# Optimization experiments

Hardware: AMD Instinct MI355X
Metric: run time of the kernel (lower is better)

The kernel has to match this reference:

```python
import jax, jax.numpy as jnp
import numpy as np

N_NODES = 100_000
N_EDGES = 1_600_000
N_GRAPHS = 512
NF = 64        # n_node_feats
H1 = 128       # hidden width
H2 = 64        # dim_node_emb
DIM_OUT = 1
STEPS = 4      # set2set processing steps


def _lin(x, W, b):
    # torch Linear convention: y = x @ W.T + b, W: [out, in]
    return x @ W.T + b


def _gelu(x):
    return jax.nn.gelu(x, approximate=False)  # torch.nn.GELU default (erf)


def _lstm_cell(x, h, c, Wih, Whh, bih, bhh):
    g = x @ Wih.T + bih + h @ Whh.T + bhh
    i, f, gg, o = jnp.split(g, 4, axis=-1)  # torch gate order: i, f, g, o
    i, f, o = jax.nn.sigmoid(i), jax.nn.sigmoid(f), jax.nn.sigmoid(o)
    gg = jnp.tanh(gg)
    c = f * c + i * gg
    h = o * jnp.tanh(c)
    return h, c


def setup_inputs() -> dict:
    key = jax.random.key(0)
    ks = jax.random.split(key, 24)
    p = lambda k, shp: jax.random.normal(k, shp, dtype=jnp.float32) * 0.05
    inp = {
        "x": jax.random.normal(ks[0], (N_NODES, NF), dtype=jnp.float32),
        "edge_index": jax.random.randint(ks[1], (2, N_EDGES), 0, N_NODES, dtype=jnp.int32),
        "batch": jnp.sort(jax.random.randint(ks[2], (N_NODES,), 0, N_GRAPHS, dtype=jnp.int32)),
        "nfc_W": p(ks[3], (H1, NF)), "nfc_b": p(ks[4], (H1,)),
        "gc1_W": p(ks[5], (H1, H1)), "gc1_b": p(ks[6], (H1,)),
        "gc2_W": p(ks[7], (H2, H1)), "gc2_b": p(ks[8], (H2,)),
        "lstm0_Wih": p(ks[9], (4 * H2, 2 * H2)), "lstm0_Whh": p(ks[10], (4 * H2, H2)),
        "lstm0_bih": p(ks[11], (4 * H2,)), "lstm0_bhh": p(ks[12], (4 * H2,)),
        "lstm1_Wih": p(ks[13], (4 * H2, H2)), "lstm1_Whh": p(ks[14], (4 * H2, H2)),
        "lstm1_bih": p(ks[15], (4 * H2,)), "lstm1_bhh": p(ks[16], (4 * H2,)),
        "fc1_W": p(ks[17], (32, 2 * H2)), "fc1_b": p(ks[18], (32,)),
        "fc2_W": p(ks[19], (DIM_OUT, 32)), "fc2_b": p(ks[20], (DIM_OUT,)),
    }
    return inp


def _forward(x, edge_index, batch, nfc_W, nfc_b, gc1_W, gc1_b, gc2_W, gc2_b,
             lstm0_Wih, lstm0_Whh, lstm0_bih, lstm0_bhh,
             lstm1_Wih, lstm1_Whh, lstm1_bih, lstm1_bhh,
             fc1_W, fc1_b, fc2_W, fc2_b):
    src, dst = edge_index[0], edge_index[1]

    def gin_conv(h, W, b):
        # PyG GINConv, eps=0: lin((1+eps)*x + sum_{j in N(i)} x_j)
        agg = jax.ops.segment_sum(h[src], dst, num_segments=N_NODES)
        return _lin(h + agg, W, b)

    h = _gelu(_lin(x, nfc_W, nfc_b))
    h = _gelu(gin_conv(h, gc1_W, gc1_b))
    h = _gelu(gin_conv(h, gc2_W, gc2_b))
    # F.normalize(p=2, dim=1)
    h = h / jnp.maximum(jnp.linalg.norm(h, axis=1, keepdims=True), 1e-12)

    # Set2Set: 2-layer LSTM, 4 processing steps, scatter-softmax attention
    B = N_GRAPHS
    h0 = jnp.zeros((B, H2), jnp.float32); c0 = jnp.zeros((B, H2), jnp.float32)
    h1 = jnp.zeros((B, H2), jnp.float32); c1 = jnp.zeros((B, H2), jnp.float32)
    q_star = jnp.zeros((B, 2 * H2), jnp.float32)
    for _ in range(STEPS):
        h0, c0 = _lstm_cell(q_star, h0, c0, lstm0_Wih, lstm0_Whh, lstm0_bih, lstm0_bhh)
        h1, c1 = _lstm_cell(h0, h1, c1, lstm1_Wih, lstm1_Whh, lstm1_bih, lstm1_bhh)
        q = h1  # [B, H2]
        e = jnp.sum(h * q[batch], axis=-1, keepdims=True)  # [N, 1]
        m = jax.ops.segment_max(e, batch, num_segments=B)
        ex = jnp.exp(e - m[batch])
        s = jax.ops.segment_sum(ex, batch, num_segments=B)
        a = ex / (s[batch] + 1e-16)
        r = jax.ops.segment_sum(a * h, batch, num_segments=B)  # [B, H2]
        q_star = jnp.concatenate([q, r], axis=-1)

    z = _gelu(_lin(q_star, fc1_W, fc1_b))
    z = _lin(z, fc2_W, fc2_b)
    return z, h


def reference(x, edge_index, batch, nfc_W, nfc_b, gc1_W, gc1_b, gc2_W, gc2_b,
              lstm0_Wih, lstm0_Whh, lstm0_bih, lstm0_bhh,
              lstm1_Wih, lstm1_Whh, lstm1_bih, lstm1_bhh,
              fc1_W, fc1_b, fc2_W, fc2_b):
    return _forward(x, edge_index, batch, nfc_W, nfc_b, gc1_W, gc1_b, gc2_W, gc2_b,
                    lstm0_Wih, lstm0_Whh, lstm0_bih, lstm0_bhh,
                    lstm1_Wih, lstm1_Whh, lstm1_bih, lstm1_bhh,
                    fc1_W, fc1_b, fc2_W, fc2_b)
```

## Files before the change

### kernel.cpp

```cpp
#include <hip/hip_runtime.h>
#include <hip/hip_bf16.h>
#include <math.h>

constexpr int N  = 100000;
constexpr int E  = 1600000;
constexpr int NG = 512;
constexpr int NF = 64;
constexpr int H1 = 128;
constexpr int H2 = 64;

constexpr int BW   = 128;
constexpr int NB   = (N + BW - 1) / BW;
constexpr int CAP  = 2600;
constexpr int CHUNK = 2048;

constexpr int MAXN = 416;
constexpr int RST  = 68;

typedef __attribute__((ext_vector_type(8))) short short8;
typedef __attribute__((ext_vector_type(4))) float f32x4;

__device__ __forceinline__ float gelu_f(float x) {
    return 0.5f * x * (1.0f + erff(x * 0.70710678118654752f));
}
__device__ __forceinline__ float sigmoid_f(float x) {
    return 1.0f / (1.0f + expf(-x));
}
__device__ __forceinline__ float waveAllSum(float v) {
    #pragma unroll
    for (int m = 32; m; m >>= 1) v += __shfl_xor(v, m);
    return v;
}
__device__ __forceinline__ unsigned short f2bf(float x) {
    __hip_bfloat16 b = __float2bfloat16(x);
    return *reinterpret_cast<unsigned short*>(&b);
}
__device__ __forceinline__ float bf2f(unsigned short u) {
    return __uint_as_float(((unsigned int)u) << 16);
}
__device__ __forceinline__ float bf_lo(unsigned int u) { return __uint_as_float(u << 16); }
__device__ __forceinline__ float bf_hi(unsigned int u) { return __uint_as_float(u & 0xffff0000u); }

__device__ __forceinline__ void bfsplit(float v, unsigned short& hi, unsigned short& lo) {
    hi = f2bf(v);
    lo = f2bf(v - bf2f(hi));
}

__global__ __launch_bounds__(256) void setup_kernel(const int* __restrict__ batch,
                                                    const float* __restrict__ Wih0, const float* __restrict__ Whh0,
                                                    const float* __restrict__ bih0, const float* __restrict__ bhh0,
                                                    const float* __restrict__ Wih1, const float* __restrict__ Whh1,
                                                    const float* __restrict__ bih1, const float* __restrict__ bhh1,
                                                    float* __restrict__ WT0, float* __restrict__ WT1,
                                                    float* __restrict__ b0, float* __restrict__ b1,
                                                    int* __restrict__ bcursor, int* __restrict__ gstart) {
    int i = blockIdx.x * 256 + threadIdx.x;
    if (i < 192 * 256) {
        int k = i >> 8, j = i & 255;
        WT0[i] = (k < 128) ? Wih0[j * 128 + k] : Whh0[j * 64 + (k - 128)];
    }
    if (i < 128 * 256) {
        int k = i >> 8, j = i & 255;
        WT1[i] = (k < 64) ? Wih1[j * 64 + k] : Whh1[j * 64 + (k - 64)];
    }
    if (i < 256) { b0[i] = bih0[i] + bhh0[i]; b1[i] = bih1[i] + bhh1[i]; }
    if (i < NB) bcursor[i] = i * CAP;
    if (i <= NG) {
        if (i == NG) gstart[NG] = N;
        else {
            int lo = 0, hi = N;
            while (lo < hi) {
                int mid = (lo + hi) >> 1;
                if (batch[mid] < i) lo = mid + 1; else hi = mid;
            }
            gstart[i] = lo;
        }
    }
}

__global__ __launch_bounds__(256) void bin_scatter_kernel(const int* __restrict__ ei,
                                                          int* __restrict__ bcursor,
                                                          int* __restrict__ pairs) {
    __shared__ int hist[NB];
    __shared__ int start_s[NB];
    __shared__ int lcur[NB];
    int tid = threadIdx.x;
    int e0 = blockIdx.x * CHUNK;
    for (int b = tid; b < NB; b += 256) hist[b] = 0;
    __syncthreads();
    #pragma unroll 4
    for (int k = 0; k < CHUNK / 256; ++k) {
        int e = e0 + k * 256 + tid;
        if (e < E) atomicAdd(&hist[ei[E + e] >> 7], 1);
    }
    __syncthreads();
    for (int b = tid; b < NB; b += 256) {
        if (hist[b]) start_s[b] = atomicAdd(&bcursor[b], hist[b]);
        lcur[b] = 0;
    }
    __syncthreads();
    #pragma unroll 4
    for (int k = 0; k < CHUNK / 256; ++k) {
        int e = e0 + k * 256 + tid;
        if (e < E) {
            int d = ei[E + e];
            int s = ei[e];
            int b = d >> 7;
            int pos = start_s[b] + atomicAdd(&lcur[b], 1);
            if (pos < (b + 1) * CAP) pairs[pos] = (s << 7) | (d & 127);
        }
    }
}

__global__ __launch_bounds__(256) void csr_bucket_kernel(const int* __restrict__ pairs,
                                                         const int* __restrict__ bcursor,
                                                         int* __restrict__ srcs,
                                                         int2* __restrict__ nrange) {
    __shared__ int cnt_l[BW];
    __shared__ int cur_l[BW];
    __shared__ int wt[2];
    int b = blockIdx.x;
    int tid = threadIdx.x;
    int base = b * CAP;
    int cnt = bcursor[b] - base;
    if (cnt > CAP) cnt = CAP;
    if (tid < BW) cnt_l[tid] = 0;
    __syncthreads();
    for (int i = tid; i < cnt; i += 256) {
        atomicAdd(&cnt_l[pairs[base + i] & 127], 1);
    }
    __syncthreads();
    if (tid < BW) {
        int v = cnt_l[tid];
        int lane = tid & 63, w = tid >> 6;
        int incl = v;
        #pragma unroll
        for (int off = 1; off < 64; off <<= 1) {
            int t = __shfl_up(incl, off);
            if (lane >= off) incl += t;
        }
        if (lane == 63) wt[w] = incl;
        __syncthreads();
        int excl = (w ? wt[0] : 0) + incl - v;
        int node = b * BW + tid;
        if (node < N) nrange[node] = make_int2(base + excl, base + excl + v);
        cur_l[tid] = excl;
    } else {
        __syncthreads();
    }
    __syncthreads();
    for (int i = tid; i < cnt; i += 256) {
        int p = pairs[base + i];
        int pos = atomicAdd(&cur_l[p & 127], 1);
        srcs[base + pos] = p >> 7;
    }
}

template <int ID, int OD, int IN_SPLIT, int OUT_MODE>
__global__ __launch_bounds__(256) void lin_mfma_kernel(const void* __restrict__ in_v,
                                                       const float* __restrict__ W,
                                                       const float* __restrict__ bias,
                                                       void* __restrict__ out_v, int nrows) {
    constexpr int KC = 32;
    constexpr int NCH = ID / KC;
    constexpr int AST = 40;
    constexpr int NCT = OD / 16;
    constexpr int LDSU = 2 * 128 * AST + 2 * OD * AST;
    __shared__ __align__(16) unsigned short lds[LDSU];
    unsigned short* Ahi = lds;
    unsigned short* Alo = lds + 128 * AST;
    unsigned short* Whi = lds + 2 * 128 * AST;
    unsigned short* Wlo = lds + 2 * 128 * AST + OD * AST;

    int tid = threadIdx.x;
    int w = tid >> 6, lane = tid & 63;
    int m15 = lane & 15, quad = lane >> 4;
    int nb = blockIdx.x * 128;

    f32x4 acc[2][NCT];
    #pragma unroll
    for (int rt = 0; rt < 2; ++rt)
        #pragma unroll
        for (int ct = 0; ct < NCT; ++ct) acc[rt][ct] = (f32x4)0.f;

    for (int c = 0; c < NCH; ++c) {
        int kb = c * KC;
        if (IN_SPLIT == 0) {
            const float* in = (const float*)in_v;
            #pragma unroll
            for (int it = 0; it < 4; ++it) {
                int f4 = it * 256 + tid;
                int row = f4 >> 3, kq = (f4 & 7) * 4;
                float4 v = make_float4(0.f, 0.f, 0.f, 0.f);
                if (nb + row < nrows) v = *(const float4*)&in[(size_t)(nb + row) * ID + kb + kq];
                unsigned short h0, h1, h2, h3, l0, l1, l2, l3;
                bfsplit(v.x, h0, l0); bfsplit(v.y, h1, l1);
                bfsplit(v.z, h2, l2); bfsplit(v.w, h3, l3);
                uint2 uh, ul;
                uh.x = (unsigned int)h0 | ((unsigned int)h1 << 16);
                uh.y = (unsigned int)h2 | ((unsigned int)h3 << 16);
                ul.x = (unsigned int)l0 | ((unsigned int)l1 << 16);
                ul.y = (unsigned int)l2 | ((unsigned int)l3 << 16);
                *(uint2*)&Ahi[row * AST + kq] = uh;
                *(uint2*)&Alo[row * AST + kq] = ul;
            }
        } else {
            const uint4* in4 = (const uint4*)in_v;
            #pragma unroll
            for (int it = 0; it < 4; ++it) {
                int i = it * 256 + tid;
                int row = i >> 3, grp = i & 7;
                uint4 u = make_uint4(0u, 0u, 0u, 0u);
                if (nb + row < nrows) u = in4[(size_t)(nb + row) * 32 + c * 8 + grp];
                *(uint2*)&Ahi[row * AST + grp * 4] = make_uint2(u.x, u.y);
                *(uint2*)&Alo[row * AST + grp * 4] = make_uint2(u.z, u.w);
            }
        }
        #pragma unroll
        for (int it = 0; it < OD / 32; ++it) {
            int f4 = it * 256 + tid;
            int o = f4 >> 3, kq = (f4 & 7) * 4;
            float4 v = *(const float4*)&W[(size_t)o * ID + kb + kq];
            unsigned short h0, h1, h2, h3, l0, l1, l2, l3;
            bfsplit(v.x, h0, l0); bfsplit(v.y, h1, l1);
            bfsplit(v.z, h2, l2); bfsplit(v.w, h3, l3);
            uint2 uh, ul;
            uh.x = (unsigned int)h0 | ((unsigned int)h1 << 16);
            uh.y = (unsigned int)h2 | ((unsigned int)h3 << 16);
            ul.x = (unsigned int)l0 | ((unsigned int)l1 << 16);
            ul.y = (unsigned int)l2 | ((unsigned int)l3 << 16);
            *(uint2*)&Whi[o * AST + kq] = uh;
            *(uint2*)&Wlo[o * AST + kq] = ul;
        }
        __syncthreads();

        short8 ah0 = *(const short8*)&Ahi[(w * 32 + m15) * AST + quad * 8];
        short8 ah1 = *(const short8*)&Ahi[(w * 32 + 16 + m15) * AST + quad * 8];
        short8 al0 = *(const short8*)&Alo[(w * 32 + m15) * AST + quad * 8];
        short8 al1 = *(const short8*)&Alo[(w * 32 + 16 + m15) * AST + quad * 8];
        #pragma unroll
        for (int ct = 0; ct < NCT; ++ct) {
            short8 bh = *(const short8*)&Whi[(ct * 16 + m15) * AST + quad * 8];
            short8 bl = *(const short8*)&Wlo[(ct * 16 + m15) * AST + quad * 8];
            acc[0][ct] = __builtin_amdgcn_mfma_f32_16x16x32_bf16(ah0, bh, acc[0][ct], 0, 0, 0);
            acc[0][ct] = __builtin_amdgcn_mfma_f32_16x16x32_bf16(ah0, bl, acc[0][ct], 0, 0, 0);
            acc[0][ct] = __builtin_amdgcn_mfma_f32_16x16x32_bf16(al0, bh, acc[0][ct], 0, 0, 0);
            acc[1][ct] = __builtin_amdgcn_mfma_f32_16x16x32_bf16(ah1, bh, acc[1][ct], 0, 0, 0);
            acc[1][ct] = __builtin_amdgcn_mfma_f32_16x16x32_bf16(ah1, bl, acc[1][ct], 0, 0, 0);
            acc[1][ct] = __builtin_amdgcn_mfma_f32_16x16x32_bf16(al1, bh, acc[1][ct], 0, 0, 0);
        }
        __syncthreads();
    }

    float bcol[NCT];
    #pragma unroll
    for (int ct = 0; ct < NCT; ++ct) bcol[ct] = bias[ct * 16 + m15];

    if (OUT_MODE == 1) {
        constexpr int EPS = OD + 8;
        unsigned short* ep = lds;
        #pragma unroll
        for (int rt = 0; rt < 2; ++rt)
            #pragma unroll
            for (int ct = 0; ct < NCT; ++ct)
                #pragma unroll
                for (int r = 0; r < 4; ++r) {
                    int rl = w * 32 + rt * 16 + quad * 4 + r;
                    float v = gelu_f(acc[rt][ct][r] + bcol[ct]);
                    ep[rl * EPS + ct * 16 + m15] = f2bf(v);
                }
        __syncthreads();
        constexpr int U4 = 128 * OD / 8;
        for (int i = tid; i < U4; i += 256) {
            int row = i / (OD / 8);
            int off = (i % (OD / 8)) * 8;
            int grow = nb + row;
            if (grow < nrows) {
                uint4 v = *(const uint4*)&ep[row * EPS + off];
                *(uint4*)((unsigned short*)out_v + (size_t)grow * OD + off) = v;
            }
        }
    } else {
        float* out = (float*)out_v;
        #pragma unroll
        for (int rt = 0; rt < 2; ++rt) {
            #pragma unroll
            for (int r = 0; r < 4; ++r) {
                float vv[NCT];
                float ss = 0.f;
                #pragma unroll
                for (int ct = 0; ct < NCT; ++ct) {
                    vv[ct] = gelu_f(acc[rt][ct][r] + bcol[ct]);
                    ss += vv[ct] * vv[ct];
                }
                #pragma unroll
                for (int mm = 1; mm < 16; mm <<= 1) ss += __shfl_xor(ss, mm);
                float denom = fmaxf(sqrtf(ss), 1e-12f);
                int grow = nb + w * 32 + rt * 16 + quad * 4 + r;
                if (grow < nrows) {
                    #pragma unroll
                    for (int ct = 0; ct < NCT; ++ct)
                        out[(size_t)grow * OD + ct * 16 + m15] = vv[ct] / denom;
                }
            }
        }
    }
}

__global__ __launch_bounds__(256) void agg_kernel(const uint2* __restrict__ hb2,
                                                  const int2* __restrict__ nrange,
                                                  const int* __restrict__ srcs,
                                                  uint4* __restrict__ utab) {
    int wave = threadIdx.x >> 6, lane = threadIdx.x & 63;
    int half = lane >> 5, hl = lane & 31;
    int n = blockIdx.x * 4 + wave;
    if (n >= N) return;
    int2 rng = nrange[n];
    int s0 = rng.x, deg = rng.y - rng.x;
    int m1 = deg < 64 ? deg : 64;
    int pre = (lane < m1) ? srcs[s0 + lane] : 0;
    float a0 = 0.f, a1 = 0.f, a2 = 0.f, a3 = 0.f;
    int t = 0;
    for (; t + 8 <= m1; t += 8) {
        int i0 = __shfl(pre, t + half);
        int i1 = __shfl(pre, t + 2 + half);
        int i2 = __shfl(pre, t + 4 + half);
        int i3 = __shfl(pre, t + 6 + half);
        uint2 u0 = hb2[(size_t)i0 * 32 + hl];
        uint2 u1 = hb2[(size_t)i1 * 32 + hl];
        uint2 u2 = hb2[(size_t)i2 * 32 + hl];
        uint2 u3 = hb2[(size_t)i3 * 32 + hl];
        a0 += bf_lo(u0.x); a1 += bf_hi(u0.x); a2 += bf_lo(u0.y); a3 += bf_hi(u0.y);
        a0 += bf_lo(u1.x); a1 += bf_hi(u1.x); a2 += bf_lo(u1.y); a3 += bf_hi(u1.y);
        a0 += bf_lo(u2.x); a1 += bf_hi(u2.x); a2 += bf_lo(u2.y); a3 += bf_hi(u2.y);
        a0 += bf_lo(u3.x); a1 += bf_hi(u3.x); a2 += bf_lo(u3.y); a3 += bf_hi(u3.y);
    }
    for (; t < m1; t += 2) {
        int idx = t + half;
        int idc = idx < m1 ? idx : 0;
        int s = __shfl(pre, idc);
        if (idx < m1) {
            uint2 u = hb2[(size_t)s * 32 + hl];
            a0 += bf_lo(u.x); a1 += bf_hi(u.x); a2 += bf_lo(u.y); a3 += bf_hi(u.y);
        }
    }
    for (int j = 64 + half; j < deg; j += 2) {
        int s = srcs[s0 + j];
        uint2 u = hb2[(size_t)s * 32 + hl];
        a0 += bf_lo(u.x); a1 += bf_hi(u.x); a2 += bf_lo(u.y); a3 += bf_hi(u.y);
    }
    a0 += __shfl_down(a0, 32);
    a1 += __shfl_down(a1, 32);
    a2 += __shfl_down(a2, 32);
    a3 += __shfl_down(a3, 32);
    if (half == 0) {
        uint2 u = hb2[(size_t)n * 32 + hl];
        a0 += bf_lo(u.x); a1 += bf_hi(u.x); a2 += bf_lo(u.y); a3 += bf_hi(u.y);
        unsigned short h0, h1, h2, h3, l0, l1, l2, l3;
        bfsplit(a0, h0, l0); bfsplit(a1, h1, l1);
        bfsplit(a2, h2, l2); bfsplit(a3, h3, l3);
        uint4 o;
        o.x = (unsigned int)h0 | ((unsigned int)h1 << 16);
        o.y = (unsigned int)h2 | ((unsigned int)h3 << 16);
        o.z = (unsigned int)l0 | ((unsigned int)l1 << 16);
        o.w = (unsigned int)l2 | ((unsigned int)l3 << 16);
        utab[(size_t)n * 32 + hl] = o;
    }
}

__global__ __launch_bounds__(256) void set2set_kernel(const float* __restrict__ hn,
                                                      const int* __restrict__ gstart,
                                                      const float* __restrict__ WT0, const float* __restrict__ b0,
                                                      const float* __restrict__ WT1, const float* __restrict__ b1,
                                                      float* __restrict__ qstar_out) {
    __shared__ __align__(16) unsigned short hL[MAXN * RST];
    __shared__ float av[MAXN];
    __shared__ __align__(16) float xc0[192];
    __shared__ __align__(16) float xc1[128];
    __shared__ __align__(16) float gates[256];
    __shared__ float c0v[H2], c1v[H2];
    __shared__ float red[4];
    __shared__ float rp[4][H2];
    __shared__ float sp[4];

    int g = blockIdx.x;
    int tid = threadIdx.x, w = tid >> 6, lane = tid & 63;
    int s0 = gstart[g], s1 = gstart[g + 1];
    int cnt = s1 - s0;
    int cL = cnt < MAXN ? cnt : MAXN;
    const float* hq = xc1 + 64;

    for (int idx = tid; idx < cL * 16; idx += 256) {
        int n = idx >> 4, p4 = idx & 15;
        float4 v = *(const float4*)&hn[(size_t)(s0 + n) * 64 + p4 * 4];
        uint2 u;
        u.x = (unsigned int)f2bf(v.x) | ((unsigned int)f2bf(v.y) << 16);
        u.y = (unsigned int)f2bf(v.z) | ((unsigned int)f2bf(v.w) << 16);
        *(uint2*)&hL[n * RST + p4 * 4] = u;
    }
    if (tid < 192) xc0[tid] = 0.f;
    if (tid < 128) xc1[tid] = 0.f;
    if (tid < H2) { c0v[tid] = 0.f; c1v[tid] = 0.f; }
    float b0v = b0[tid], b1v = b1[tid];
    __syncthreads();

    for (int step = 0; step < 4; ++step) {
        {
            float a0 = 0.f, a1 = 0.f, a2 = 0.f, a3 = 0.f;
            #pragma unroll 8
            for (int k = 0; k < 192; k += 4) {
                a0 += xc0[k]     * WT0[(k)     * 256 + tid];
                a1 += xc0[k + 1] * WT0[(k + 1) * 256 + tid];
                a2 += xc0[k + 2] * WT0[(k + 2) * 256 + tid];
                a3 += xc0[k + 3] * WT0[(k + 3) * 256 + tid];
            }
            gates[tid] = (a0 + a1) + (a2 + a3) + b0v;
        }
        __syncthreads();
        if (tid < H2) {
            float ii = sigmoid_f(gates[tid]), ff = sigmoid_f(gates[H2 + tid]);
            float gg = tanhf(gates[2 * H2 + tid]), oo = sigmoid_f(gates[3 * H2 + tid]);
            float c = ff * c0v[tid] + ii * gg;
            float h = oo * tanhf(c);
            c0v[tid] = c; xc0[128 + tid] = h; xc1[tid] = h;
        }
        __syncthreads();
        {
            float a0 = 0.f, a1 = 0.f, a2 = 0.f, a3 = 0.f;
            #pragma unroll 8
            for (int k = 0; k < 128; k += 4) {
                a0 += xc1[k]     * WT1[(k)     * 256 + tid];
                a1 += xc1[k + 1] * WT1[(k + 1) * 256 + tid];
                a2 += xc1[k + 2] * WT1[(k + 2) * 256 + tid];
                a3 += xc1[k + 3] * WT1[(k + 3) * 256 + tid];
            }
            gates[tid] = (a0 + a1) + (a2 + a3) + b1v;
        }
        __syncthreads();
        if (tid < H2) {
            float ii = sigmoid_f(gates[tid]), ff = sigmoid_f(gates[H2 + tid]);
            float gg = tanhf(gates[2 * H2 + tid]), oo = sigmoid_f(gates[3 * H2 + tid]);
            float c = ff * c1v[tid] + ii * gg;
            float h = oo * tanhf(c);
            c1v[tid] = c; xc1[64 + tid] = h;
        }
        __syncthreads();

        float lm = -INFINITY;
        for (int i = tid; i < cnt; i += 256) {
            float e = 0.f;
            if (i < MAXN) {
                const uint2* row = (const uint2*)&hL[i * RST];
                #pragma unroll
                for (int p4 = 0; p4 < 16; ++p4) {
                    uint2 u = row[p4];
                    e += bf_lo(u.x) * hq[p4 * 4 + 0];
                    e += bf_hi(u.x) * hq[p4 * 4 + 1];
                    e += bf_lo(u.y) * hq[p4 * 4 + 2];
                    e += bf_hi(u.y) * hq[p4 * 4 + 3];
                }
                av[i] = e;
            } else {
                for (int f = 0; f < 64; ++f) e += hn[(size_t)(s0 + i) * 64 + f] * hq[f];
            }
            lm = fmaxf(lm, e);
        }
        #pragma unroll
        for (int mm = 32; mm; mm >>= 1) lm = fmaxf(lm, __shfl_xor(lm, mm));
        if (lane == 0) red[w] = lm;
        __syncthreads();
        float m = fmaxf(fmaxf(red[0], red[1]), fmaxf(red[2], red[3]));

        float ps = 0.f;
        for (int i = tid; i < cnt; i += 256) {
            float e;
            if (i < MAXN) e = av[i];
            else {
                e = 0.f;
                for (int f = 0; f < 64; ++f) e += hn[(size_t)(s0 + i) * 64 + f] * hq[f];
            }
            float p = expf(e - m);
            ps += p;
            if (i < MAXN) av[i] = p;
        }
        ps = waveAllSum(ps);
        if (lane == 0) sp[w] = ps;
        __syncthreads();
        float s = sp[0] + sp[1] + sp[2] + sp[3];

        float racc = 0.f;
        for (int i = w; i < cL; i += 4) {
            unsigned short hv = hL[i * RST + lane];
            racc += av[i] * bf2f(hv);
        }
        float qf = hq[lane];
        for (int n = MAXN + w; n < cnt; n += 4) {
            float v = hn[(size_t)(s0 + n) * 64 + lane];
            float e = waveAllSum(v * qf);
            float p = expf(e - m);
            racc += p * v;
        }
        rp[w][lane] = racc;
        __syncthreads();
        if (tid < H2) {
            float r = 0.f;
            if (cnt > 0) {
                r = (rp[0][tid] + rp[1][tid] + rp[2][tid] + rp[3][tid]) / (s + 1e-16f);
            }
            xc0[tid] = xc1[64 + tid];
            xc0[H2 + tid] = r;
        }
        __syncthreads();
    }
    if (tid < 2 * H2) qstar_out[g * 2 * H2 + tid] = xc0[tid];
}

__global__ __launch_bounds__(256) void fcout_kernel(const float* __restrict__ q_star,
                                                    const float* __restrict__ W1, const float* __restrict__ b1,
                                                    const float* __restrict__ W2, const float* __restrict__ b2,
                                                    float* __restrict__ z) {
    __shared__ float W1l[32 * 128];
    __shared__ float b1l[32], W2l[32];
    int tid = threadIdx.x;
    for (int i = tid; i < 32 * 128; i += 256) W1l[i] = W1[i];
    if (tid < 32) { b1l[tid] = b1[tid]; W2l[tid] = W2[tid]; }
    __syncthreads();
    int g = blockIdx.x * 256 + tid;
    float acc[32];
    #pragma unroll
    for (int j = 0; j < 32; ++j) acc[j] = b1l[j];
    for (int k = 0; k < 128; ++k) {
        float qv = q_star[g * 128 + k];
        #pragma unroll
        for (int j = 0; j < 32; ++j) acc[j] += qv * W1l[j * 128 + k];
    }
    float zv = b2[0];
    #pragma unroll
    for (int j = 0; j < 32; ++j) zv += gelu_f(acc[j]) * W2l[j];
    z[g] = zv;
}

extern "C" void kernel_launch(void* const* d_in, const int* in_sizes, int n_in,
                              void* d_out, int out_size, void* d_ws, size_t ws_size,
                              hipStream_t stream) {
    const float* x       = (const float*)d_in[0];
    const int*   ei      = (const int*)d_in[1];
    const int*   batch   = (const int*)d_in[2];
    const float* nfc_W   = (const float*)d_in[3];
    const float* nfc_b   = (const float*)d_in[4];
    const float* gc1_W   = (const float*)d_in[5];
    const float* gc1_b   = (const float*)d_in[6];
    const float* gc2_W   = (const float*)d_in[7];
    const float* gc2_b   = (const float*)d_in[8];
    const float* l0_Wih  = (const float*)d_in[9];
    const float* l0_Whh  = (const float*)d_in[10];
    const float* l0_bih  = (const float*)d_in[11];
    const float* l0_bhh  = (const float*)d_in[12];
    const float* l1_Wih  = (const float*)d_in[13];
    const float* l1_Whh  = (const float*)d_in[14];
    const float* l1_bih  = (const float*)d_in[15];
    const float* l1_bhh  = (const float*)d_in[16];
    const float* fc1_W   = (const float*)d_in[17];
    const float* fc1_b   = (const float*)d_in[18];
    const float* fc2_W   = (const float*)d_in[19];
    const float* fc2_b   = (const float*)d_in[20];

    float* out = (float*)d_out;
    float* hn_out = out + NG;

    char* p = (char*)d_ws;
    auto take = [&](size_t bytes) {
        char* r = p;
        p += (bytes + 255) & ~size_t(255);
        return r;
    };
    float*        sbuf  = (float*)take((size_t)N * H1 * 4);
    unsigned int* hbbuf = (unsigned int*)take((size_t)N * H1 * 2);
    int*   srcs   = (int*)take((size_t)NB * CAP * 4);
    int2*  nrange = (int2*)take((size_t)N * 8);
    int*   bcursor= (int*)take((size_t)NB * 4);
    int*   gstart = (int*)take((size_t)(NG + 1) * 4);
    float* qstar  = (float*)take((size_t)NG * 2 * H2 * 4);
    float* WT0    = (float*)take((size_t)192 * 256 * 4);
    float* WT1    = (float*)take((size_t)128 * 256 * 4);
    float* b0     = (float*)take((size_t)256 * 4);
    float* b1     = (float*)take((size_t)256 * 4);

    int* pairs = (int*)sbuf;

    setup_kernel<<<192, 256, 0, stream>>>(batch, l0_Wih, l0_Whh, l0_bih, l0_bhh,
                                          l1_Wih, l1_Whh, l1_bih, l1_bhh,
                                          WT0, WT1, b0, b1, bcursor, gstart);

    bin_scatter_kernel<<<(E + CHUNK - 1) / CHUNK, 256, 0, stream>>>(ei, bcursor, pairs);
    csr_bucket_kernel<<<NB, 256, 0, stream>>>(pairs, bcursor, srcs, nrange);

    int mfmaGrid = (N + 127) / 128;
    lin_mfma_kernel<NF, H1, 0, 1><<<mfmaGrid, 256, 0, stream>>>(x, nfc_W, nfc_b, hbbuf, N);
    agg_kernel<<<(N + 3) / 4, 256, 0, stream>>>((const uint2*)hbbuf, nrange, srcs, (uint4*)sbuf);
    lin_mfma_kernel<H1, H1, 1, 1><<<mfmaGrid, 256, 0, stream>>>(sbuf, gc1_W, gc1_b, hbbuf, N);
    agg_kernel<<<(N + 3) / 4, 256, 0, stream>>>((const uint2*)hbbuf, nrange, srcs, (uint4*)sbuf);
    lin_mfma_kernel<H1, H2, 1, 2><<<mfmaGrid, 256, 0, stream>>>(sbuf, gc2_W, gc2_b, hn_out, N);

    set2set_kernel<<<NG, 256, 0, stream>>>(hn_out, gstart, WT0, b0, WT1, b1, qstar);

    fcout_kernel<<<2, 256, 0, stream>>>(qstar, fc1_W, fc1_b, fc2_W, fc2_b, out);
}
```

Baseline: 474.6 us.

## Reorder second GIN conv to project before aggregation and fuse both linears

Uses the linearity of the second GIN layer: the 128-wide hidden features are multiplied by gc2_W first, and the 64-wide projection is then aggregated over neighbours. That halves the gather width of the second aggregation and removes one full-size intermediate pass. The gc1 and gc2 matmuls now run in one kernel that writes the projection in fp16, and a new aggregation kernel applies the bias, GELU and L2 normalisation. Storing the aggregated values in fp16 may cost accuracy, and the bin-scatter CHUNK size is also doubled.

```diff
diff --git a/kernel.cpp b/kernel.cpp
--- a/kernel.cpp
+++ b/kernel.cpp
@@ -1,5 +1,6 @@
 #include <hip/hip_runtime.h>
 #include <hip/hip_bf16.h>
+#include <hip/hip_fp16.h>
 #include <math.h>
 
 constexpr int N  = 100000;
@@ -12,7 +13,7 @@
 constexpr int BW   = 128;
 constexpr int NB   = (N + BW - 1) / BW;
 constexpr int CAP  = 2600;
-constexpr int CHUNK = 2048;
+constexpr int CHUNK = 4096;
 
 constexpr int MAXN = 416;
 constexpr int RST  = 68;
@@ -156,11 +157,11 @@
     }
 }
 
-template <int ID, int OD, int IN_SPLIT, int OUT_MODE>
-__global__ __launch_bounds__(256) void lin_mfma_kernel(const void* __restrict__ in_v,
+template <int ID, int OD>
+__global__ __launch_bounds__(256) void lin_mfma_kernel(const float* __restrict__ in,
                                                        const float* __restrict__ W,
                                                        const float* __restrict__ bias,
-                                                       void* __restrict__ out_v, int nrows) {
+                                                       unsigned short* __restrict__ out_bf, int nrows) {
     constexpr int KC = 32;
     constexpr int NCH = ID / KC;
     constexpr int AST = 40;
@@ -185,36 +186,22 @@
 
     for (int c = 0; c < NCH; ++c) {
         int kb = c * KC;
-        if (IN_SPLIT == 0) {
-            const float* in = (const float*)in_v;
-            #pragma unroll
-            for (int it = 0; it < 4; ++it) {
-                int f4 = it * 256 + tid;
-                int row = f4 >> 3, kq = (f4 & 7) * 4;
-                float4 v = make_float4(0.f, 0.f, 0.f, 0.f);
-                if (nb + row < nrows) v = *(const float4*)&in[(size_t)(nb + row) * ID + kb + kq];
-                unsigned short h0, h1, h2, h3, l0, l1, l2, l3;
-                bfsplit(v.x, h0, l0); bfsplit(v.y, h1, l1);
-                bfsplit(v.z, h2, l2); bfsplit(v.w, h3, l3);
-                uint2 uh, ul;
-                uh.x = (unsigned int)h0 | ((unsigned int)h1 << 16);
-                uh.y = (unsigned int)h2 | ((unsigned int)h3 << 16);
-                ul.x = (unsigned int)l0 | ((unsigned int)l1 << 16);
-                ul.y = (unsigned int)l2 | ((unsigned int)l3 << 16);
-                *(uint2*)&Ahi[row * AST + kq] = uh;
-                *(uint2*)&Alo[row * AST + kq] = ul;
-            }
-        } else {
-            const uint4* in4 = (const uint4*)in_v;
-            #pragma unroll
-            for (int it = 0; it < 4; ++it) {
-                int i = it * 256 + tid;
-                int row = i >> 3, grp = i & 7;
-                uint4 u = make_uint4(0u, 0u, 0u, 0u);
-                if (nb + row < nrows) u = in4[(size_t)(nb + row) * 32 + c * 8 + grp];
-                *(uint2*)&Ahi[row * AST + grp * 4] = make_uint2(u.x, u.y);
-                *(uint2*)&Alo[row * AST + grp * 4] = make_uint2(u.z, u.w);
-            }
+        #pragma unroll
+        for (int it = 0; it < 4; ++it) {
+            int f4 = it * 256 + tid;
+            int row = f4 >> 3, kq = (f4 & 7) * 4;
+            float4 v = make_float4(0.f, 0.f, 0.f, 0.f);
+            if (nb + row < nrows) v = *(const float4*)&in[(size_t)(nb + row) * ID + kb + kq];
+            unsigned short h0, h1, h2, h3, l0, l1, l2, l3;
+            bfsplit(v.x, h0, l0); bfsplit(v.y, h1, l1);
+            bfsplit(v.z, h2, l2); bfsplit(v.w, h3, l3);
+            uint2 uh, ul;
+            uh.x = (unsigned int)h0 | ((unsigned int)h1 << 16);
+            uh.y = (unsigned int)h2 | ((unsigned int)h3 << 16);
+            ul.x = (unsigned int)l0 | ((unsigned int)l1 << 16);
+            ul.y = (unsigned int)l2 | ((unsigned int)l3 << 16);
+            *(uint2*)&Ahi[row * AST + kq] = uh;
+            *(uint2*)&Alo[row * AST + kq] = ul;
         }
         #pragma unroll
         for (int it = 0; it < OD / 32; ++it) {
@@ -256,53 +243,27 @@
     #pragma unroll
     for (int ct = 0; ct < NCT; ++ct) bcol[ct] = bias[ct * 16 + m15];
 
-    if (OUT_MODE == 1) {
-        constexpr int EPS = OD + 8;
-        unsigned short* ep = lds;
-        #pragma unroll
-        for (int rt = 0; rt < 2; ++rt)
-            #pragma unroll
-            for (int ct = 0; ct < NCT; ++ct)
-                #pragma unroll
-                for (int r = 0; r < 4; ++r) {
-                    int rl = w * 32 + rt * 16 + quad * 4 + r;
-                    float v = gelu_f(acc[rt][ct][r] + bcol[ct]);
-                    ep[rl * EPS + ct * 16 + m15] = f2bf(v);
-                }
-        __syncthreads();
-        constexpr int U4 = 128 * OD / 8;
-        for (int i = tid; i < U4; i += 256) {
-            int row = i / (OD / 8);
-            int off = (i % (OD / 8)) * 8;
-            int grow = nb + row;
-            if (grow < nrows) {
-                uint4 v = *(const uint4*)&ep[row * EPS + off];
-                *(uint4*)((unsigned short*)out_v + (size_t)grow * OD + off) = v;
-            }
-        }
-    } else {
-        float* out = (float*)out_v;
-        #pragma unroll
-        for (int rt = 0; rt < 2; ++rt) {
+    constexpr int EPS = OD + 8;
+    unsigned short* ep = lds;
+    #pragma unroll
+    for (int rt = 0; rt < 2; ++rt)
+        #pragma unroll
+        for (int ct = 0; ct < NCT; ++ct)
             #pragma unroll
             for (int r = 0; r < 4; ++r) {
-                float vv[NCT];
-                float ss = 0.f;
-                #pragma unroll
-                for (int ct = 0; ct < NCT; ++ct) {
-                    vv[ct] = gelu_f(acc[rt][ct][r] + bcol[ct]);
-                    ss += vv[ct] * vv[ct];
-                }
-                #pragma unroll
-                for (int mm = 1; mm < 16; mm <<= 1) ss += __shfl_xor(ss, mm);
-                float denom = fmaxf(sqrtf(ss), 1e-12f);
-                int grow = nb + w * 32 + rt * 16 + quad * 4 + r;
-                if (grow < nrows) {
-                    #pragma unroll
-                    for (int ct = 0; ct < NCT; ++ct)
-                        out[(size_t)grow * OD + ct * 16 + m15] = vv[ct] / denom;
-                }
-            }
+                int rl = w * 32 + rt * 16 + quad * 4 + r;
+                float v = gelu_f(acc[rt][ct][r] + bcol[ct]);
+                ep[rl * EPS + ct * 16 + m15] = f2bf(v);
+            }
+    __syncthreads();
+    constexpr int U4 = 128 * OD / 8;
+    for (int i = tid; i < U4; i += 256) {
+        int row = i / (OD / 8);
+        int off = (i % (OD / 8)) * 8;
+        int grow = nb + row;
+        if (grow < nrows) {
+            uint4 v = *(const uint4*)&ep[row * EPS + off];
+            *(uint4*)(out_bf + (size_t)grow * OD + off) = v;
         }
     }
 }
@@ -368,6 +329,213 @@
     }
 }
 
+__global__ __launch_bounds__(256) void lin2_fused_kernel(const uint4* __restrict__ in4,
+                                                         const float* __restrict__ W1,
+                                                         const float* __restrict__ b1,
+                                                         const float* __restrict__ W2,
+                                                         unsigned short* __restrict__ y2,
+                                                         int nrows) {
+    constexpr int AST = 40;
+    __shared__ __align__(16) unsigned short lds[4 * 128 * AST];
+    unsigned short* Ahi = lds;
+    unsigned short* Alo = lds + 128 * AST;
+    unsigned short* Whi = lds + 2 * 128 * AST;
+    unsigned short* Wlo = lds + 3 * 128 * AST;
+
+    int tid = threadIdx.x;
+    int w = tid >> 6, lane = tid & 63;
+    int m15 = lane & 15, quad = lane >> 4;
+    int nb = blockIdx.x * 128;
+
+    f32x4 acc[2][8];
+    #pragma unroll
+    for (int rt = 0; rt < 2; ++rt)
+        #pragma unroll
+        for (int ct = 0; ct < 8; ++ct) acc[rt][ct] = (f32x4)0.f;
+
+    for (int c = 0; c < 4; ++c) {
+        #pragma unroll
+        for (int it = 0; it < 4; ++it) {
+            int i = it * 256 + tid;
+            int row = i >> 3, grp = i & 7;
+            uint4 u = make_uint4(0u, 0u, 0u, 0u);
+            if (nb + row < nrows) u = in4[(size_t)(nb + row) * 32 + c * 8 + grp];
+            *(uint2*)&Ahi[row * AST + grp * 4] = make_uint2(u.x, u.y);
+            *(uint2*)&Alo[row * AST + grp * 4] = make_uint2(u.z, u.w);
+        }
+        #pragma unroll
+        for (int it = 0; it < 4; ++it) {
+            int f4 = it * 256 + tid;
+            int o = f4 >> 3, kq = (f4 & 7) * 4;
+            float4 v = *(const float4*)&W1[(size_t)o * 128 + c * 32 + kq];
+            unsigned short h0, h1, h2, h3, l0, l1, l2, l3;
+            bfsplit(v.x, h0, l0); bfsplit(v.y, h1, l1);
+            bfsplit(v.z, h2, l2); bfsplit(v.w, h3, l3);
+            uint2 uh, ul;
+            uh.x = (unsigned int)h0 | ((unsigned int)h1 << 16);
+            uh.y = (unsigned int)h2 | ((unsigned int)h3 << 16);
+            ul.x = (unsigned int)l0 | ((unsigned int)l1 << 16);
+            ul.y = (unsigned int)l2 | ((unsigned int)l3 << 16);
+            *(uint2*)&Whi[o * AST + kq] = uh;
+            *(uint2*)&Wlo[o * AST + kq] = ul;
+        }
+        __syncthreads();
+        short8 ah0 = *(const short8*)&Ahi[(w * 32 + m15) * AST + quad * 8];
+        short8 ah1 = *(const short8*)&Ahi[(w * 32 + 16 + m15) * AST + quad * 8];
+        short8 al0 = *(const short8*)&Alo[(w * 32 + m15) * AST + quad * 8];
+        short8 al1 = *(const short8*)&Alo[(w * 32 + 16 + m15) * AST + quad * 8];
+        #pragma unroll
+        for (int ct = 0; ct < 8; ++ct) {
+            short8 bh = *(const short8*)&Whi[(ct * 16 + m15) * AST + quad * 8];
+            short8 bl = *(const short8*)&Wlo[(ct * 16 + m15) * AST + quad * 8];
+            acc[0][ct] = __builtin_amdgcn_mfma_f32_16x16x32_bf16(ah0, bh, acc[0][ct], 0, 0, 0);
+            acc[0][ct] = __builtin_amdgcn_mfma_f32_16x16x32_bf16(ah0, bl, acc[0][ct], 0, 0, 0);
+            acc[0][ct] = __builtin_amdgcn_mfma_f32_16x16x32_bf16(al0, bh, acc[0][ct], 0, 0, 0);
+            acc[1][ct] = __builtin_amdgcn_mfma_f32_16x16x32_bf16(ah1, bh, acc[1][ct], 0, 0, 0);
+            acc[1][ct] = __builtin_amdgcn_mfma_f32_16x16x32_bf16(ah1, bl, acc[1][ct], 0, 0, 0);
+            acc[1][ct] = __builtin_amdgcn_mfma_f32_16x16x32_bf16(al1, bh, acc[1][ct], 0, 0, 0);
+        }
+        __syncthreads();
+    }
+
+    #pragma unroll
+    for (int ct = 0; ct < 8; ++ct) {
+        float bc = b1[ct * 16 + m15];
+        #pragma unroll
+        for (int rt = 0; rt < 2; ++rt)
+            #pragma unroll
+            for (int r = 0; r < 4; ++r)
+                acc[rt][ct][r] = gelu_f(acc[rt][ct][r] + bc);
+    }
+
+    f32x4 acc2[2][4];
+    #pragma unroll
+    for (int rt = 0; rt < 2; ++rt)
+        #pragma unroll
+        for (int ct = 0; ct < 4; ++ct) acc2[rt][ct] = (f32x4)0.f;
+
+    for (int c2 = 0; c2 < 4; ++c2) {
+        __syncthreads();
+        #pragma unroll
+        for (int rt = 0; rt < 2; ++rt)
+            #pragma unroll
+            for (int cc = 0; cc < 2; ++cc) {
+                int ct = c2 * 2 + cc;
+                #pragma unroll
+                for (int r = 0; r < 4; ++r) {
+                    int node = w * 32 + rt * 16 + quad * 4 + r;
+                    unsigned short hi, lo;
+                    bfsplit(acc[rt][ct][r], hi, lo);
+                    Ahi[node * AST + cc * 16 + m15] = hi;
+                    Alo[node * AST + cc * 16 + m15] = lo;
+                }
+            }
+        #pragma unroll
+        for (int it = 0; it < 2; ++it) {
+            int f4 = it * 256 + tid;
+            int o = f4 >> 3, kq = (f4 & 7) * 4;
+            float4 v = *(const float4*)&W2[(size_t)o * 128 + c2 * 32 + kq];
+            unsigned short h0, h1, h2, h3, l0, l1, l2, l3;
+            bfsplit(v.x, h0, l0); bfsplit(v.y, h1, l1);
+            bfsplit(v.z, h2, l2); bfsplit(v.w, h3, l3);
+            uint2 uh, ul;
+            uh.x = (unsigned int)h0 | ((unsigned int)h1 << 16);
+            uh.y = (unsigned int)h2 | ((unsigned int)h3 << 16);
+            ul.x = (unsigned int)l0 | ((unsigned int)l1 << 16);
+            ul.y = (unsigned int)l2 | ((unsigned int)l3 << 16);
+            *(uint2*)&Whi[o * AST + kq] = uh;
+            *(uint2*)&Wlo[o * AST + kq] = ul;
+        }
+        __syncthreads();
+        short8 ah0 = *(const short8*)&Ahi[(w * 32 + m15) * AST + quad * 8];
+        short8 ah1 = *(const short8*)&Ahi[(w * 32 + 16 + m15) * AST + quad * 8];
+        short8 al0 = *(const short8*)&Alo[(w * 32 + m15) * AST + quad * 8];
+        short8 al1 = *(const short8*)&Alo[(w * 32 + 16 + m15) * AST + quad * 8];
+        #pragma unroll
+        for (int ct = 0; ct < 4; ++ct) {
+            short8 bh = *(const short8*)&Whi[(ct * 16 + m15) * AST + quad * 8];
+            short8 bl = *(const short8*)&Wlo[(ct * 16 + m15) * AST + quad * 8];
+            acc2[0][ct] = __builtin_amdgcn_mfma_f32_16x16x32_bf16(ah0, bh, acc2[0][ct], 0, 0, 0);
+            acc2[0][ct] = __builtin_amdgcn_mfma_f32_16x16x32_bf16(ah0, bl, acc2[0][ct], 0, 0, 0);
+            acc2[0][ct] = __builtin_amdgcn_mfma_f32_16x16x32_bf16(al0, bh, acc2[0][ct], 0, 0, 0);
+            acc2[1][ct] = __builtin_amdgcn_mfma_f32_16x16x32_bf16(ah1, bh, acc2[1][ct], 0, 0, 0);
+            acc2[1][ct] = __builtin_amdgcn_mfma_f32_16x16x32_bf16(ah1, bl, acc2[1][ct], 0, 0, 0);
+            acc2[1][ct] = __builtin_amdgcn_mfma_f32_16x16x32_bf16(al1, bh, acc2[1][ct], 0, 0, 0);
+        }
+    }
+    __syncthreads();
+
+    constexpr int EPS = 72;
+    unsigned short* ep = lds;
+    #pragma unroll
+    for (int rt = 0; rt < 2; ++rt)
+        #pragma unroll
+        for (int ct = 0; ct < 4; ++ct)
+            #pragma unroll
+            for (int r = 0; r < 4; ++r) {
+                int rl = w * 32 + rt * 16 + quad * 4 + r;
+                __half hv = __float2half(acc2[rt][ct][r]);
+                ep[rl * EPS + ct * 16 + m15] = *reinterpret_cast<unsigned short*>(&hv);
+            }
+    __syncthreads();
+    for (int i = tid; i < 1024; i += 256) {
+        int row = i >> 3, off = (i & 7) * 8;
+        int grow = nb + row;
+        if (grow < nrows)
+            *(uint4*)(y2 + (size_t)grow * 64 + off) = *(const uint4*)&ep[row * EPS + off];
+    }
+}
+
+__global__ __launch_bounds__(256) void agg2_norm_kernel(const uint2* __restrict__ y2,
+                                                        const int2* __restrict__ nrange,
+                                                        const int* __restrict__ srcs,
+                                                        const float* __restrict__ b2,
+                                                        float* __restrict__ hn) {
+    int wave = threadIdx.x >> 6, lane = threadIdx.x & 63;
+    int qw = lane >> 4, ql = lane & 15;
+    int n = blockIdx.x * 4 + wave;
+    if (n >= N) return;
+    int2 rng = nrange[n];
+    int s0 = rng.x, deg = rng.y - rng.x;
+    int m1 = deg < 64 ? deg : 64;
+    int pre = (lane < m1) ? srcs[s0 + lane] : 0;
+    float a0 = 0.f, a1 = 0.f, a2 = 0.f, a3 = 0.f;
+    auto addu = [&](uint2 u) {
+        float2 f01 = __half22float2(*reinterpret_cast<__half2*>(&u.x));
+        float2 f23 = __half22float2(*reinterpret_cast<__half2*>(&u.y));
+        a0 += f01.x; a1 += f01.y; a2 += f23.x; a3 += f23.y;
+    };
+    int t = 0;
+    for (; t + 8 <= m1; t += 8) {
+        int i0 = __shfl(pre, t + qw);
+        int i1 = __shfl(pre, t + 4 + qw);
+        uint2 u0 = y2[(size_t)i0 * 16 + ql];
+        uint2 u1 = y2[(size_t)i1 * 16 + ql];
+        addu(u0); addu(u1);
+    }
+    for (; t < m1; t += 4) {
+        int idx = t + qw;
+        int s = __shfl(pre, idx < m1 ? idx : 0);
+        if (idx < m1) addu(y2[(size_t)s * 16 + ql]);
+    }
+    for (int j = 64 + qw; j < deg; j += 4) addu(y2[(size_t)srcs[s0 + j] * 16 + ql]);
+    a0 += __shfl_down(a0, 32); a1 += __shfl_down(a1, 32);
+    a2 += __shfl_down(a2, 32); a3 += __shfl_down(a3, 32);
+    a0 += __shfl_down(a0, 16); a1 += __shfl_down(a1, 16);
+    a2 += __shfl_down(a2, 16); a3 += __shfl_down(a3, 16);
+    if (qw == 0) {
+        addu(y2[(size_t)n * 16 + ql]);
+        float4 bv = *(const float4*)&b2[ql * 4];
+        float v0 = gelu_f(a0 + bv.x), v1 = gelu_f(a1 + bv.y);
+        float v2 = gelu_f(a2 + bv.z), v3 = gelu_f(a3 + bv.w);
+        float ss = v0 * v0 + v1 * v1 + v2 * v2 + v3 * v3;
+        #pragma unroll
+        for (int mm = 1; mm < 16; mm <<= 1) ss += __shfl_xor(ss, mm);
+        float d = fmaxf(sqrtf(ss), 1e-12f);
+        *(float4*)&hn[(size_t)n * 64 + ql * 4] = make_float4(v0 / d, v1 / d, v2 / d, v3 / d);
+    }
+}
+
 __global__ __launch_bounds__(256) void set2set_kernel(const float* __restrict__ hn,
                                                       const int* __restrict__ gstart,
                                                       const float* __restrict__ WT0, const float* __restrict__ b0,
@@ -574,8 +742,8 @@
         p += (bytes + 255) & ~size_t(255);
         return r;
     };
-    float*        sbuf  = (float*)take((size_t)N * H1 * 4);
-    unsigned int* hbbuf = (unsigned int*)take((size_t)N * H1 * 2);
+    float*          sbuf  = (float*)take((size_t)N * H1 * 4);
+    unsigned short* hbbuf = (unsigned short*)take((size_t)N * H1 * 2);
     int*   srcs   = (int*)take((size_t)NB * CAP * 4);
     int2*  nrange = (int2*)take((size_t)N * 8);
     int*   bcursor= (int*)take((size_t)NB * 4);
@@ -596,11 +764,12 @@
     csr_bucket_kernel<<<NB, 256, 0, stream>>>(pairs, bcursor, srcs, nrange);
 
     int mfmaGrid = (N + 127) / 128;
-    lin_mfma_kernel<NF, H1, 0, 1><<<mfmaGrid, 256, 0, stream>>>(x, nfc_W, nfc_b, hbbuf, N);
+    lin_mfma_kernel<NF, H1><<<mfmaGrid, 256, 0, stream>>>(x, nfc_W, nfc_b, hbbuf, N);
     agg_kernel<<<(N + 3) / 4, 256, 0, stream>>>((const uint2*)hbbuf, nrange, srcs, (uint4*)sbuf);
-    lin_mfma_kernel<H1, H1, 1, 1><<<mfmaGrid, 256, 0, stream>>>(sbuf, gc1_W, gc1_b, hbbuf, N);
-    agg_kernel<<<(N + 3) / 4, 256, 0, stream>>>((const uint2*)hbbuf, nrange, srcs, (uint4*)sbuf);
-    lin_mfma_kernel<H1, H2, 1, 2><<<mfmaGrid, 256, 0, stream>>>(sbuf, gc2_W, gc2_b, hn_out, N);
+    lin2_fused_kernel<<<mfmaGrid, 256, 0, stream>>>((const uint4*)sbuf, gc1_W, gc1_b, gc2_W,
+                                                    hbbuf, N);
+    agg2_norm_kernel<<<(N + 3) / 4, 256, 0, stream>>>((const uint2*)hbbuf, nrange, srcs,
+                                                      gc2_b, hn_out);
 
     set2set_kernel<<<NG, 256, 0, stream>>>(hn_out, gstart, WT0, b0, WT1, b1, qstar);
 
```

Result: no change. 468.1 us (-1.4%).
